# Performance work log

Measured on AMD Instinct MI355X. Metric: run time of the kernel, lower is better.

The kernel has to match this reference:

```python
import jax, jax.numpy as jnp
import numpy as np

STRIDES = (8, 16, 32)
SIZES = ((80, 80), (40, 40), (20, 20))  # 640x640 input
PRE_TOP_K = 1000
KEEP_TOP_K = 100
IOU_THR = 0.65
SCORE_THR = 0.25
CLASS_OFFSET = 4096.0  # > max image extent, for class-aware NMS


def setup_inputs() -> dict:
    key = jax.random.key(0)
    ks = jax.random.split(key, 6)
    B, C = 8, 1203
    d = {}
    for i, (h, w) in enumerate(SIZES):
        d[f"cls_scores_{i}"] = jax.random.normal(ks[i], (B, C, h, w), dtype=jnp.float32)
        d[f"bbox_preds_{i}"] = jax.random.uniform(ks[3 + i], (B, 4, h, w), dtype=jnp.float32)
    return d


def _flatten(feats, ch):
    B = feats[0].shape[0]
    return jnp.concatenate([f.transpose(0, 2, 3, 1).reshape(B, -1, ch) for f in feats], axis=1)


def _priors():
    pts, strs = [], []
    for (h, w), s in zip(SIZES, STRIDES):
        yy, xx = jnp.meshgrid(jnp.arange(h, dtype=jnp.float32), jnp.arange(w, dtype=jnp.float32), indexing="ij")
        pts.append(jnp.stack([(xx.ravel() + 0.5) * s, (yy.ravel() + 0.5) * s], axis=-1))
        strs.append(jnp.full((h * w,), float(s), dtype=jnp.float32))
    return jnp.concatenate(pts, 0), jnp.concatenate(strs, 0)


def _decode(priors, preds, stride):
    # DistancePointBBoxCoder: preds are LTRB distances scaled by stride.
    d = preds * stride[None, :, None]  # [B,N,4]
    x1 = priors[None, :, 0] - d[..., 0]
    y1 = priors[None, :, 1] - d[..., 1]
    x2 = priors[None, :, 0] + d[..., 2]
    y2 = priors[None, :, 1] + d[..., 3]
    return jnp.stack([x1, y1, x2, y2], axis=-1)


def _iou_matrix(b):
    area = (b[:, 2] - b[:, 0]) * (b[:, 3] - b[:, 1])
    lt = jnp.maximum(b[:, None, :2], b[None, :, :2])
    rb = jnp.minimum(b[:, None, 2:], b[None, :, 2:])
    wh = jnp.clip(rb - lt, 0.0)
    inter = wh[..., 0] * wh[..., 1]
    return inter / (area[:, None] + area[None, :] - inter + 1e-7)


def _nms_single(boxes, scores, labels):
    # boxes [N,4], scores [N] (max over classes), labels [N] int
    ts, idx = jax.lax.top_k(scores, PRE_TOP_K)
    b = boxes[idx]
    l = labels[idx]
    valid = ts > SCORE_THR
    off = b + (l.astype(b.dtype) * CLASS_OFFSET)[:, None]  # class-aware trick
    iou = _iou_matrix(off)  # [K,K]

    def body(keep, i):
        suppressed = jnp.any(keep & (iou[:, i] > IOU_THR))
        keep = keep.at[i].set(valid[i] & ~suppressed)
        return keep, None

    keep, _ = jax.lax.scan(body, jnp.zeros((PRE_TOP_K,), bool), jnp.arange(PRE_TOP_K))
    kept_scores = jnp.where(keep, ts, -1.0)
    fs, fi = jax.lax.top_k(kept_scores, KEEP_TOP_K)
    m = fs > 0.0
    det_boxes = jnp.where(m[:, None], b[fi], 0.0)
    det_scores = jnp.where(m, fs, 0.0)
    det_labels = jnp.where(m, l[fi], -1)
    num_dets = m.sum().astype(jnp.int32)
    return num_dets, det_boxes, det_scores, det_labels


def reference(cls_scores_0, cls_scores_1, cls_scores_2, bbox_preds_0, bbox_preds_1, bbox_preds_2):
    C = cls_scores_0.shape[1]
    cls_scores = jax.nn.sigmoid(_flatten([cls_scores_0, cls_scores_1, cls_scores_2], C))  # [B,N,C]
    preds = _flatten([bbox_preds_0, bbox_preds_1, bbox_preds_2], 4)  # [B,N,4]
    priors, stride = _priors()
    boxes = _decode(priors, preds, stride)  # [B,N,4]
    max_scores = cls_scores.max(axis=-1)  # [B,N]
    labels = cls_scores.argmax(axis=-1)  # [B,N]
    num_dets, det_boxes, det_scores, det_labels = jax.vmap(_nms_single)(boxes, max_scores, labels)
    return num_dets, det_boxes, det_scores, det_labels
```

## Files before the change

kernel.cpp:

```cpp
#include <hip/hip_runtime.h>
#include <math.h>

#pragma clang fp contract(off)

typedef unsigned long long u64;
typedef unsigned int u32;
typedef float f4 __attribute__((ext_vector_type(4)));
typedef unsigned long long u64x2 __attribute__((ext_vector_type(2)));

#define BB 8
#define CC_TOT 1203
#define NANC 8400
#define NSEL 1000
#define NCAND 1024
#define NT 1024
#define NBATCH 128
#define NCHUNK_MAX 16

__device__ __forceinline__ u32 okey32(float v) {
  u32 b = __float_as_uint(v);
  return (b & 0x80000000u) ? ~b : (b | 0x80000000u);
}

__device__ __forceinline__ float unokey32(u32 ok) {
  u32 fb = (ok & 0x80000000u) ? (ok & 0x7FFFFFFFu) : ~ok;
  return __uint_as_float(fb);
}

__global__ __launch_bounds__(256) void kmax(const float* __restrict__ cls0,
                                            const float* __restrict__ cls1,
                                            const float* __restrict__ cls2,
                                            u64* __restrict__ part,
                                            int chunkSz, int nchunk) {
  int bx = blockIdx.x;
  int per = nchunk * BB;
  int tg = bx / per;
  int rem = bx - tg * per;
  int chunk = rem >> 3;
  int b = rem & 7;
  const float* cls; int hw4, aoff, col0;
  if (tg < 7)      { cls = cls0; hw4 = 1600; aoff = 0;    col0 = tg << 8; }
  else if (tg < 9) { cls = cls1; hw4 = 400;  aoff = 6400; col0 = (tg - 7) << 8; }
  else             { cls = cls2; hw4 = 100;  aoff = 8000; col0 = 0; }
  int col = col0 + (int)threadIdx.x;
  if (col >= hw4) return;
  int c0 = chunk * chunkSz;
  int c1 = c0 + chunkSz; if (c1 > CC_TOT) c1 = CC_TOT;

  const f4* base = (const f4*)cls + (size_t)b * CC_TOT * hw4 + col;
  f4 m = (f4){-3.4e38f, -3.4e38f, -3.4e38f, -3.4e38f};
  int ix0 = c0, ix1 = c0, ix2 = c0, ix3 = c0;

#define UPD(v, c)                                   \
  do {                                              \
    if ((v)[0] > m[0]) { m[0] = (v)[0]; ix0 = (c); } \
    if ((v)[1] > m[1]) { m[1] = (v)[1]; ix1 = (c); } \
    if ((v)[2] > m[2]) { m[2] = (v)[2]; ix2 = (c); } \
    if ((v)[3] > m[3]) { m[3] = (v)[3]; ix3 = (c); } \
  } while (0)

  int c = c0;
  for (; c + 8 <= c1; c += 8) {
    const f4* p = base + (size_t)c * hw4;
    f4 v0 = p[0];
    f4 v1 = p[(size_t)1 * hw4];
    f4 v2 = p[(size_t)2 * hw4];
    f4 v3 = p[(size_t)3 * hw4];
    f4 v4 = p[(size_t)4 * hw4];
    f4 v5 = p[(size_t)5 * hw4];
    f4 v6 = p[(size_t)6 * hw4];
    f4 v7 = p[(size_t)7 * hw4];
    UPD(v0, c + 0); UPD(v1, c + 1); UPD(v2, c + 2); UPD(v3, c + 3);
    UPD(v4, c + 4); UPD(v5, c + 5); UPD(v6, c + 6); UPD(v7, c + 7);
  }
  for (; c < c1; ++c) {
    f4 v = base[(size_t)c * hw4];
    UPD(v, c);
  }
#undef UPD

  u64* dst = part + ((size_t)chunk * BB + b) * NANC + aoff + (size_t)col * 4;
  u64x2 s01 = { ((u64)okey32(m[0]) << 32) | (u64)(u32)~(u32)ix0,
                ((u64)okey32(m[1]) << 32) | (u64)(u32)~(u32)ix1 };
  u64x2 s23 = { ((u64)okey32(m[2]) << 32) | (u64)(u32)~(u32)ix2,
                ((u64)okey32(m[3]) << 32) | (u64)(u32)~(u32)ix3 };
  *((u64x2*)dst)     = s01;
  *((u64x2*)dst + 1) = s23;
}

__global__ __launch_bounds__(256) void kreduce(const u64* __restrict__ part,
                                               u64* __restrict__ fin, int nchunk) {
  int a = blockIdx.x * 256 + threadIdx.x;
  if (a >= NANC) return;
  int b = blockIdx.y;
  size_t off = (size_t)b * NANC + a;
  const size_t PL = (size_t)BB * NANC;
  const u64* p = part + off;
  u64 m = p[0];
  int ch = 1;
  for (; ch + 4 <= nchunk; ch += 4) {
    u64 v0 = p[(size_t)(ch + 0) * PL];
    u64 v1 = p[(size_t)(ch + 1) * PL];
    u64 v2 = p[(size_t)(ch + 2) * PL];
    u64 v3 = p[(size_t)(ch + 3) * PL];
    u64 a01 = (v0 > v1) ? v0 : v1;
    u64 a23 = (v2 > v3) ? v2 : v3;
    u64 a03 = (a01 > a23) ? a01 : a23;
    m = (a03 > m) ? a03 : m;
  }
  for (; ch < nchunk; ++ch) {
    u64 v = p[(size_t)ch * PL];
    m = (v > m) ? v : m;
  }
  u32 lab = ~(u32)m;
  fin[off] = (m & 0xFFFFFFFF00000000ull) | ((u64)(u32)(0xFFFFu - (u32)a) << 16) | (u64)(lab & 0xFFFFu);
}

struct DecodeArrays {
  float xo1[NCAND], yo1[NCAND], xo2[NCAND], yo2[NCAND], ar[NCAND];
  float rx1[NCAND], ry1[NCAND], rx2[NCAND], ry2[NCAND], sc[NCAND];
  int lab[NCAND], val[NCAND];
};

__device__ __forceinline__ void hist_add_clustered(u32* hist, u32 digit, int lane) {
  u64 peers = ~0ull;
  for (int bit = 0; bit < 13; ++bit) {
    u64 bal = __ballot((digit >> bit) & 1u);
    peers &= ((digit >> bit) & 1u) ? bal : ~bal;
  }
  int leader = __ffsll((unsigned long long)peers) - 1;
  if (digit < 4096u && lane == leader)
    atomicAdd(&hist[digit], (u32)__popcll((unsigned long long)peers));
}

__device__ __forceinline__ void suffix_pick(u32* hist, u32* waveTot, u32* waveSufExcl,
                                            u64* prefixSh, u32* rankSh,
                                            u64 prefix, u32 rank, int shift,
                                            int tid, int lane, int wv) {
  u32 l0 = hist[4 * tid], l1 = hist[4 * tid + 1], l2 = hist[4 * tid + 2], l3 = hist[4 * tid + 3];
  u32 psum = l0 + l1 + l2 + l3;
  u32 x = psum;
  for (int s = 1; s < 64; s <<= 1) { u32 v = __shfl_down(x, s); if (lane + s < 64) x += v; }
  if (lane == 0) waveTot[wv] = x;
  __syncthreads();
  if (tid < 16) {
    u32 y = waveTot[tid]; u32 z = y;
    for (int s = 1; s < 16; s <<= 1) { u32 v = __shfl_down(z, s); if (tid + s < 16) z += v; }
    waveSufExcl[tid] = z - y;
  }
  __syncthreads();
  u32 S = x + waveSufExcl[wv];
  u32 G3 = S - psum; u32 G2 = G3 + l3; u32 G1 = G2 + l2; u32 G0 = G1 + l1;
  u32 r = rank;
  if      (G3 < r && G3 + l3 >= r) { *prefixSh = prefix | ((u64)(4u * tid + 3) << shift); *rankSh = r - G3; }
  else if (G2 < r && G2 + l2 >= r) { *prefixSh = prefix | ((u64)(4u * tid + 2) << shift); *rankSh = r - G2; }
  else if (G1 < r && G1 + l1 >= r) { *prefixSh = prefix | ((u64)(4u * tid + 1) << shift); *rankSh = r - G1; }
  else if (G0 < r && G0 + l0 >= r) { *prefixSh = prefix | ((u64)(4u * tid + 0) << shift); *rankSh = r - G0; }
}

__device__ __forceinline__ u64 radix_select(const u64* keys, int n, u32 target,
                                            u32* hist, u32* waveTot, u32* waveSufExcl,
                                            u64* prefixSh, u32* rankSh,
                                            int tid, int lane, int wv) {
  u64 prefix = 0; u32 rank = target;
  for (int pass = 3; pass >= 0; --pass) {
    int shift = 16 + pass * 12;
    for (int i = tid; i < 4096; i += NT) hist[i] = 0;
    __syncthreads();
    u64 hiMask = (pass == 3) ? 0ull : ((~0ull) << (shift + 12));
    if (pass == 3) {
      for (int i = tid; i < n; i += NT) {
        u64 k = keys[i];
        hist_add_clustered(hist, (u32)((k >> shift) & 4095u), lane);
      }
    } else {
      for (int i = tid; i < n; i += NT) {
        u64 k = keys[i];
        if ((k & hiMask) == (prefix & hiMask))
          atomicAdd(&hist[(u32)((k >> shift) & 4095u)], 1u);
      }
    }
    __syncthreads();
    suffix_pick(hist, waveTot, waveSufExcl, prefixSh, rankSh, prefix, rank, shift, tid, lane, wv);
    __syncthreads();
    prefix = *prefixSh; rank = *rankSh;
    __syncthreads();
  }
  return prefix;
}

__device__ __forceinline__ void gather_ge(const u64* keys, int n, u64 K, u64* dst, u32* cnt,
                                          int tid, int lane, u32 bound) {
  for (int i = tid; i < n; i += NT) {
    u64 k = keys[i];
    bool sel = (k >= K);
    u64 mask = __ballot(sel);
    if (mask) {
      int leader = __ffsll((unsigned long long)mask) - 1;
      u32 basep = 0;
      if (lane == leader) basep = atomicAdd(cnt, (u32)__popcll((unsigned long long)mask));
      basep = __shfl((int)basep, leader);
      if (sel) {
        u32 pos = basep + (u32)__popcll((unsigned long long)(mask & ((1ull << lane) - 1ull)));
        if (pos < bound) dst[pos] = k;
      }
    }
  }
}

__device__ __forceinline__ void decode_into(DecodeArrays* d, int rk, u64 my, int b,
                                            const float* bb0, const float* bb1, const float* bb2) {
  int label = (int)(u32)(my & 0xFFFFull);
  int idx = 0xFFFF - (int)(u32)((my >> 16) & 0xFFFFull);
  float logit = unokey32((u32)(my >> 32));
  float sc = 1.0f / (1.0f + expf(-logit));

  int w, str, off, hwl; const float* bb;
  if (idx < 6400)      { w = 80; str = 8;  off = 0;    hwl = 6400; bb = bb0; }
  else if (idx < 8000) { w = 40; str = 16; off = 6400; hwl = 1600; bb = bb1; }
  else                 { w = 20; str = 32; off = 8000; hwl = 400;  bb = bb2; }
  int p = idx - off;
  int y = p / w;
  int x = p - y * w;
  float fs = (float)str;
  float px = ((float)x + 0.5f) * fs;
  float py = ((float)y + 0.5f) * fs;
  const float* bp = bb + (size_t)b * 4 * hwl + p;
  float t0 = bp[0] * fs;
  float t1 = bp[hwl] * fs;
  float t2 = bp[2 * hwl] * fs;
  float t3 = bp[3 * hwl] * fs;
  float x1 = px - t0, y1 = py - t1, x2 = px + t2, y2 = py + t3;
  float lo = (float)label * 4096.0f;
  float ox1 = x1 + lo, oy1 = y1 + lo, ox2 = x2 + lo, oy2 = y2 + lo;
  float area = (ox2 - ox1) * (oy2 - oy1);

  d->xo1[rk] = ox1; d->yo1[rk] = oy1; d->xo2[rk] = ox2; d->yo2[rk] = oy2; d->ar[rk] = area;
  d->rx1[rk] = x1;  d->ry1[rk] = y1;  d->rx2[rk] = x2;  d->ry2[rk] = y2;  d->sc[rk] = sc;
  d->lab[rk] = label;
  d->val[rk] = (sc > 0.25f) ? 1 : 0;
}

__device__ __forceinline__ int nms_pass(const DecodeArrays* d, int bound, int lane, int* outIdx) {
  float ax1 = 0, ay1 = 0, ax2 = 0, ay2 = 0, aar = 0; int aon = 0;
  float bx1 = 0, by1 = 0, bx2 = 0, by2 = 0, bar = 0; int bon = 0;
  int kept = 0;
  for (int i = 0; i < bound; ++i) {
    if (kept >= 100) break;
    float cx1 = d->xo1[i], cy1 = d->yo1[i], cx2 = d->xo2[i], cy2 = d->yo2[i], car = d->ar[i];
    bool sup = false;
    if (aon) {
      float ltx = fmaxf(ax1, cx1), lty = fmaxf(ay1, cy1);
      float rbx = fminf(ax2, cx2), rby = fminf(ay2, cy2);
      float wd = fmaxf(rbx - ltx, 0.0f), ht = fmaxf(rby - lty, 0.0f);
      float inter = wd * ht;
      sup = sup || ((inter / (aar + car - inter + 1e-7f)) > 0.65f);
    }
    if (bon) {
      float ltx = fmaxf(bx1, cx1), lty = fmaxf(by1, cy1);
      float rbx = fminf(bx2, cx2), rby = fminf(by2, cy2);
      float wd = fmaxf(rbx - ltx, 0.0f), ht = fmaxf(rby - lty, 0.0f);
      float inter = wd * ht;
      sup = sup || ((inter / (bar + car - inter + 1e-7f)) > 0.65f);
    }
    bool anysup = __any(sup);
    if (d->val[i] != 0 && !anysup) {
      if (kept < 64) {
        if (lane == kept) { ax1 = cx1; ay1 = cy1; ax2 = cx2; ay2 = cy2; aar = car; aon = 1; }
      } else {
        if (lane == kept - 64) { bx1 = cx1; by1 = cy1; bx2 = cx2; by2 = cy2; bar = car; bon = 1; }
      }
      if (lane == 0) outIdx[kept] = i;
      ++kept;
    }
  }
  return kept;
}

__global__ __launch_bounds__(1024) void knms(const u64* __restrict__ fin,
                                             const float* __restrict__ bb0,
                                             const float* __restrict__ bb1,
                                             const float* __restrict__ bb2,
                                             float* __restrict__ out) {
  __shared__ union ShU {
    u64 fk[NANC];
    DecodeArrays d;
  } sh;
  __shared__ u32 hist[4096];
  __shared__ u32 waveTot[16];
  __shared__ u32 waveSufExcl[16];
  __shared__ u64 prefixSh;
  __shared__ u32 rankSh;
  __shared__ u32 gcnt;
  __shared__ __align__(16) u64 cand[NCAND];
  __shared__ __align__(16) u64 candA[NBATCH];
  __shared__ int outIdx[128];
  __shared__ int keptSh;

  int b = blockIdx.x;
  int tid = threadIdx.x;
  int lane = tid & 63;
  int wv = tid >> 6;

  {
    const u64x2* fsrc = (const u64x2*)(fin + (size_t)b * NANC);
    u64x2* fdst = (u64x2*)sh.fk;
    for (int i = tid; i < NANC / 2; i += NT) fdst[i] = fsrc[i];
  }
  __syncthreads();

  u64 K2 = radix_select(sh.fk, NANC, NBATCH, hist, waveTot, waveSufExcl,
                        &prefixSh, &rankSh, tid, lane, wv);
  if (tid == 0) gcnt = 0;
  __syncthreads();
  gather_ge(sh.fk, NANC, K2, candA, &gcnt, tid, lane, NBATCH);
  __syncthreads();

  if (tid < NBATCH) {
    u64 my = candA[tid];
    int rk = 0;
    const u64x2* cav = (const u64x2*)candA;
    #pragma unroll
    for (int j2 = 0; j2 < NBATCH / 2; ++j2) {
      u64x2 p = cav[j2];
      rk += (p[0] > my) ? 1 : 0;
      rk += (p[1] > my) ? 1 : 0;
    }
    decode_into(&sh.d, rk, my, b, bb0, bb1, bb2);
  }
  __syncthreads();
  if (tid < 64) {
    int kept = nms_pass(&sh.d, NBATCH, lane, outIdx);
    if (lane == 0) keptSh = kept;
  }
  __syncthreads();

  if (keptSh < 100) {
    {
      const u64x2* fsrc = (const u64x2*)(fin + (size_t)b * NANC);
      u64x2* fdst = (u64x2*)sh.fk;
      for (int i = tid; i < NANC / 2; i += NT) fdst[i] = fsrc[i];
    }
    __syncthreads();
    u64 K = radix_select(sh.fk, NANC, NSEL, hist, waveTot, waveSufExcl,
                         &prefixSh, &rankSh, tid, lane, wv);
    if (tid == 0) gcnt = 0;
    __syncthreads();
    gather_ge(sh.fk, NANC, K, cand, &gcnt, tid, lane, NSEL);
    __syncthreads();
    if (tid < NSEL) {
      u64 my = cand[tid];
      int rk = 0;
      const u64x2* cbv = (const u64x2*)cand;
      for (int j2 = 0; j2 < NSEL / 2; ++j2) {
        u64x2 p = cbv[j2];
        rk += (p[0] > my) ? 1 : 0;
        rk += (p[1] > my) ? 1 : 0;
      }
      decode_into(&sh.d, rk, my, b, bb0, bb1, bb2);
    }
    __syncthreads();
    if (tid < 64) {
      int kept = nms_pass(&sh.d, NSEL, lane, outIdx);
      if (lane == 0) keptSh = kept;
    }
    __syncthreads();
  }

  int kept = keptSh;
  float* o_nd = out;
  float* o_box = out + BB;
  float* o_sc = out + BB + BB * 100 * 4;
  float* o_lb = out + BB + BB * 100 * 4 + BB * 100;
  if (tid == 0) o_nd[b] = (float)kept;
  if (tid < 100) {
    int s = tid;
    float v0 = 0, v1 = 0, v2 = 0, v3 = 0, sv = 0, lv = -1.0f;
    if (s < kept) {
      int i = outIdx[s];
      v0 = sh.d.rx1[i]; v1 = sh.d.ry1[i]; v2 = sh.d.rx2[i]; v3 = sh.d.ry2[i];
      sv = sh.d.sc[i]; lv = (float)sh.d.lab[i];
    }
    float* bo = o_box + ((size_t)b * 100 + s) * 4;
    bo[0] = v0; bo[1] = v1; bo[2] = v2; bo[3] = v3;
    o_sc[b * 100 + s] = sv;
    o_lb[b * 100 + s] = lv;
  }
}

extern "C" void kernel_launch(void* const* d_in, const int* in_sizes, int n_in,
                              void* d_out, int out_size, void* d_ws, size_t ws_size,
                              hipStream_t stream) {
  const float* cls0 = (const float*)d_in[0];
  const float* bb0  = (const float*)d_in[1];
  const float* cls1 = (const float*)d_in[2];
  const float* bb1  = (const float*)d_in[3];
  const float* cls2 = (const float*)d_in[4];
  const float* bb2  = (const float*)d_in[5];

  size_t planeB = (size_t)BB * NANC * sizeof(u64);
  u64* fin = (u64*)d_ws;
  u64* part;
  int nchunk;
  if (ws_size >= 2 * planeB) {
    size_t avail = (ws_size - planeB) / planeB;
    nchunk = (int)(avail < NCHUNK_MAX ? avail : NCHUNK_MAX);
    part = fin + (size_t)BB * NANC;
  } else {
    nchunk = 1;
    part = fin;
  }
  int chunkSz = (CC_TOT + nchunk - 1) / nchunk;
  nchunk = (CC_TOT + chunkSz - 1) / chunkSz;

  kmax<<<dim3(10 * nchunk * BB), dim3(256), 0, stream>>>(cls0, cls1, cls2, part, chunkSz, nchunk);
  kreduce<<<dim3((NANC + 255) / 256, BB), dim3(256), 0, stream>>>(part, fin, nchunk);
  knms<<<dim3(BB), dim3(NT), 0, stream>>>(fin, bb0, bb1, bb2, (float*)d_out);
}
```

Before: 132.0 us.

## Fuse histogram into load and precompute IoU bitmask for first NMS batch

Builds the top-digit histogram while copying keys into shared memory, then partitions keys into a definite-top set and a boundary-digit candidate set. The remaining radix passes run only over the small candidate set, with a fallback to the full radix select if it overflows. The sequential single-wave NMS pass over the 128 best boxes is replaced by a parallel IoU suppression bitmask built by all threads, followed by a serial scan in one thread. This aims to cut full-array radix passes and NMS latency, at the cost of more shared memory and a serial thread-0 loop.

```diff
diff --git a/kernel.cpp b/kernel.cpp
--- a/kernel.cpp
+++ b/kernel.cpp
@@ -291,9 +291,11 @@
   __shared__ u32 waveSufExcl[16];
   __shared__ u64 prefixSh;
   __shared__ u32 rankSh;
-  __shared__ u32 gcnt;
+  __shared__ u32 gcnt, aCnt, cCnt;
   __shared__ __align__(16) u64 cand[NCAND];
   __shared__ __align__(16) u64 candA[NBATCH];
+  __shared__ __align__(16) u32 cm[NBATCH * 4];
+  __shared__ u64 VwSh[2];
   __shared__ int outIdx[128];
   __shared__ int keptSh;
 
@@ -302,19 +304,87 @@
   int lane = tid & 63;
   int wv = tid >> 6;
 
+  for (int i = tid; i < 4096; i += NT) hist[i] = 0;
+  if (tid == 0) { aCnt = 0; cCnt = 0; }
+  __syncthreads();
   {
     const u64x2* fsrc = (const u64x2*)(fin + (size_t)b * NANC);
     u64x2* fdst = (u64x2*)sh.fk;
-    for (int i = tid; i < NANC / 2; i += NT) fdst[i] = fsrc[i];
-  }
-  __syncthreads();
-
-  u64 K2 = radix_select(sh.fk, NANC, NBATCH, hist, waveTot, waveSufExcl,
-                        &prefixSh, &rankSh, tid, lane, wv);
-  if (tid == 0) gcnt = 0;
-  __syncthreads();
-  gather_ge(sh.fk, NANC, K2, candA, &gcnt, tid, lane, NBATCH);
-  __syncthreads();
+    for (int i = tid; i < NANC / 2; i += NT) {
+      u64x2 v = fsrc[i];
+      fdst[i] = v;
+      hist_add_clustered(hist, (u32)(v[0] >> 52), lane);
+      hist_add_clustered(hist, (u32)(v[1] >> 52), lane);
+    }
+  }
+  __syncthreads();
+
+  suffix_pick(hist, waveTot, waveSufExcl, &prefixSh, &rankSh, 0ull, NBATCH, 52, tid, lane, wv);
+  __syncthreads();
+  u64 pfx3 = prefixSh; u32 r3 = rankSh;
+  u32 d3 = (u32)(pfx3 >> 52);
+  __syncthreads();
+
+  for (int i = tid; i < NANC; i += NT) {
+    u64 k = sh.fk[i];
+    u32 dig = (u32)(k >> 52);
+    bool selA = dig > d3;
+    u64 mA = __ballot(selA);
+    if (mA) {
+      int leader = __ffsll((unsigned long long)mA) - 1;
+      u32 basep = 0;
+      if (lane == leader) basep = atomicAdd(&aCnt, (u32)__popcll((unsigned long long)mA));
+      basep = __shfl((int)basep, leader);
+      if (selA) {
+        u32 pos = basep + (u32)__popcll((unsigned long long)(mA & ((1ull << lane) - 1ull)));
+        if (pos < NBATCH) candA[pos] = k;
+      }
+    }
+    bool selC = (dig == d3);
+    u64 mC = __ballot(selC);
+    if (mC) {
+      int leader = __ffsll((unsigned long long)mC) - 1;
+      u32 basep = 0;
+      if (lane == leader) basep = atomicAdd(&cCnt, (u32)__popcll((unsigned long long)mC));
+      basep = __shfl((int)basep, leader);
+      if (selC) {
+        u32 pos = basep + (u32)__popcll((unsigned long long)(mC & ((1ull << lane) - 1ull)));
+        if (pos < NCAND) cand[pos] = k;
+      }
+    }
+  }
+  __syncthreads();
+
+  u32 cnt3 = cCnt;
+  if (cnt3 <= NCAND) {
+    u64 pfx = pfx3; u32 rk = r3;
+    for (int pass = 2; pass >= 0; --pass) {
+      int shift = 16 + pass * 12;
+      for (int i = tid; i < 4096; i += NT) hist[i] = 0;
+      __syncthreads();
+      u64 hiMask = (~0ull) << (shift + 12);
+      for (int i = tid; i < (int)cnt3; i += NT) {
+        u64 k = cand[i];
+        if ((k & hiMask) == (pfx & hiMask))
+          atomicAdd(&hist[(u32)((k >> shift) & 4095u)], 1u);
+      }
+      __syncthreads();
+      suffix_pick(hist, waveTot, waveSufExcl, &prefixSh, &rankSh, pfx, rk, shift, tid, lane, wv);
+      __syncthreads();
+      pfx = prefixSh; rk = rankSh;
+      __syncthreads();
+    }
+    u64 K2 = pfx;
+    gather_ge(cand, (int)cnt3, K2, candA, &aCnt, tid, lane, NBATCH);
+    __syncthreads();
+  } else {
+    if (tid == 0) aCnt = 0;
+    __syncthreads();
+    u64 K2 = radix_select(sh.fk, NANC, NBATCH, hist, waveTot, waveSufExcl,
+                          &prefixSh, &rankSh, tid, lane, wv);
+    gather_ge(sh.fk, NANC, K2, candA, &aCnt, tid, lane, NBATCH);
+    __syncthreads();
+  }
 
   if (tid < NBATCH) {
     u64 my = candA[tid];
@@ -328,10 +398,50 @@
     }
     decode_into(&sh.d, rk, my, b, bb0, bb1, bb2);
   }
-  __syncthreads();
-  if (tid < 64) {
-    int kept = nms_pass(&sh.d, NBATCH, lane, outIdx);
-    if (lane == 0) keptSh = kept;
+  if (tid < NBATCH * 4) cm[tid] = 0;
+  __syncthreads();
+
+  if (tid < NBATCH) {
+    u64 bal = __ballot(sh.d.val[tid] != 0);
+    if (lane == 0) VwSh[tid >> 6] = bal;
+  }
+
+  {
+    int c = tid & 127;
+    int g = tid >> 7;
+    float cx1 = sh.d.xo1[c], cy1 = sh.d.yo1[c], cx2 = sh.d.xo2[c], cy2 = sh.d.yo2[c], car = sh.d.ar[c];
+    u32 bits = 0;
+    int j0 = g * 16;
+    for (int jj = 0; jj < 16; ++jj) {
+      int j = j0 + jj;
+      float ltx = fmaxf(sh.d.xo1[j], cx1), lty = fmaxf(sh.d.yo1[j], cy1);
+      float rbx = fminf(sh.d.xo2[j], cx2), rby = fminf(sh.d.yo2[j], cy2);
+      float wd = fmaxf(rbx - ltx, 0.0f), ht = fmaxf(rby - lty, 0.0f);
+      float inter = wd * ht;
+      bool sup = (inter / (sh.d.ar[j] + car - inter + 1e-7f)) > 0.65f;
+      bits |= sup ? (1u << jj) : 0u;
+    }
+    atomicOr(&cm[c * 4 + (g >> 1)], bits << ((g & 1) * 16));
+  }
+  __syncthreads();
+
+  if (tid == 0) {
+    u32 K0 = 0, K1 = 0, K2w = 0, K3 = 0;
+    u64 V0 = VwSh[0], V1 = VwSh[1];
+    int kept = 0;
+    for (int i = 0; i < NBATCH && kept < 100; ++i) {
+      const u32* c4 = &cm[i * 4];
+      u32 sup = (c4[0] & K0) | (c4[1] & K1) | (c4[2] & K2w) | (c4[3] & K3);
+      bool valid = (((i < 64) ? (V0 >> i) : (V1 >> (i - 64))) & 1ull) != 0ull;
+      if (valid && sup == 0u) {
+        if (i < 32) K0 |= 1u << i;
+        else if (i < 64) K1 |= 1u << (i - 32);
+        else if (i < 96) K2w |= 1u << (i - 64);
+        else K3 |= 1u << (i - 96);
+        outIdx[kept++] = i;
+      }
+    }
+    keptSh = kept;
   }
   __syncthreads();
 
```

After: 120.7 us. 1.09x faster.
